# Performance work log

Measured on AMD Instinct MI355X. Metric: run time of the kernel, lower is better.

## Reference

```python
import jax, jax.numpy as jnp
import numpy as np

MAX_N = 32        # mixture degree N
N_PTS = 16384     # number of scalar inputs
INIT_DECAY = 1.0


def setup_inputs() -> dict:
    key = jax.random.key(0)
    k1, _ = jax.random.split(key)
    # inputs assumed elementwise in [-1, 1]
    xs = jax.random.uniform(k1, (N_PTS,), dtype=jnp.float32, minval=-1.0, maxval=1.0)
    # learned logits param, init logits[n] = -n * init_decay (as in __init__)
    logits = -INIT_DECAY * jnp.arange(MAX_N + 1, dtype=jnp.float32)
    return {"xs": xs, "logits": logits}


def _psi(xs, logits, max_n):
    """psi(x) = concat_n sqrt(w_n) * phi_n(x); shape (P, 2*max_n+1).

    phi_0 = [1]; phi_n = [T_n(x), sqrt(1-x^2) * U_{n-1}(x)] for n>=1.
    Single linear-pass recurrence instead of per-degree recompute.
    """
    w = jax.nn.softmax(logits)          # (max_n+1,)
    sw = jnp.sqrt(w)
    xc = jnp.clip(xs, -1.0, 1.0)        # (P,)
    s = jnp.sqrt(jnp.clip(1.0 - xc * xc, 0.0))
    P = xs.shape[0]

    # T_0..T_max_n and U_0..U_max_n via one shared recurrence (fixed small loop)
    Ts = [jnp.ones_like(xc), xc]
    Us = [jnp.ones_like(xc), 2.0 * xc]
    for _ in range(2, max_n + 1):
        Ts.append(2.0 * xc * Ts[-1] - Ts[-2])
        Us.append(2.0 * xc * Us[-1] - Us[-2])
    T = jnp.stack(Ts, axis=-1)          # (P, max_n+1)
    U = jnp.stack(Us, axis=-1)          # (P, max_n+1)

    Tn = T[:, 1:]                       # T_1..T_N            (P, max_n)
    Un = U[:, :max_n]                   # U_0..U_{N-1}        (P, max_n)
    # interleave per degree: [T_n, s * U_{n-1}], weighted by sqrt(w_n)
    pair = jnp.stack([Tn, s[:, None] * Un], axis=-1)   # (P, max_n, 2)
    pair = pair * sw[1:][None, :, None]
    head = sw[0] * jnp.ones((P, 1), dtype=xs.dtype)    # sqrt(w_0) * phi_0
    return jnp.concatenate([head, pair.reshape(P, 2 * max_n)], axis=-1)


def reference(xs, logits):
    """gram(xs) = psi(xs) @ psi(xs)^T, shape (P, P)."""
    psi = _psi(xs, logits, MAX_N)       # (P, 2*MAX_N+1)
    return psi @ psi.T
```

## Files before the change

kernel.cpp:

```cpp
#include <hip/hip_runtime.h>
#include <hip/hip_bf16.h>
#include <math.h>

#define MAXN    32
#define NPTS    16384
#define RSTRIDE 64
#define BTA     32
#define BTB     256
#define NCHUNK  ((BTA + BTB) * RSTRIDE * 2 / 1024)
#define W0_OFF  (NPTS * RSTRIDE)

typedef __attribute__((ext_vector_type(8))) short         bf16x8;
typedef __attribute__((ext_vector_type(4))) float         f32x4;
typedef __attribute__((ext_vector_type(4))) unsigned int  u32x4;

__device__ inline ushort f2bf(float f) {
    union { float f; unsigned u; } v; v.f = f;
    unsigned u = v.u;
    u += 0x7FFFu + ((u >> 16) & 1u);
    return (ushort)(u >> 16);
}

__global__ __launch_bounds__(256) void psi_kernel(
    const float* __restrict__ xs, const float* __restrict__ logits,
    ushort* __restrict__ psi, float* __restrict__ w0scr)
{
    __shared__ ushort srow[256 * RSTRIDE];

    const int tid = threadIdx.x;
    const int pt  = blockIdx.x * 256 + tid;

    float x = xs[pt];
    x = fminf(1.0f, fmaxf(-1.0f, x));
    float s = sqrtf(fmaxf(0.0f, 1.0f - x * x));

    float m = -3.4e38f;
    #pragma unroll
    for (int n = 0; n <= MAXN; ++n) m = fmaxf(m, logits[n]);
    float sum = 0.0f;
    #pragma unroll
    for (int n = 0; n <= MAXN; ++n) sum += __expf(logits[n] - m);
    float inv = 1.0f / sum;

    if (pt == 0) w0scr[0] = __expf(logits[0] - m) * inv;

    ushort tmp[RSTRIDE];
    float Tm1 = 1.0f, T = x;
    float Um1 = 1.0f, U = 2.0f * x;
    float tx = 2.0f * x;
    #pragma unroll
    for (int n = 1; n <= MAXN; ++n) {
        float swn = sqrtf(__expf(logits[n] - m) * inv);
        tmp[2 * n - 2] = f2bf(swn * T);
        tmp[2 * n - 1] = f2bf(swn * (s * Um1));
        float Tn = tx * T - Tm1; Tm1 = T; T = Tn;
        float Un = tx * U - Um1; Um1 = U; U = Un;
    }

    {
        u32x4* lrow = (u32x4*)(srow + tid * RSTRIDE);
        const u32x4* src = (const u32x4*)tmp;
        const int rx = tid & 7;
        #pragma unroll
        for (int j = 0; j < 8; ++j) lrow[j ^ rx] = src[j];
    }
    __syncthreads();

    {
        const u32x4* ls = (const u32x4*)srow;
        u32x4* gd = (u32x4*)(psi + (size_t)blockIdx.x * 256 * RSTRIDE);
        #pragma unroll
        for (int i = 0; i < 8; ++i) gd[i * 256 + tid] = ls[i * 256 + tid];
    }
}

__device__ inline void load_lds16(const void* g, void* l) {
    __builtin_amdgcn_global_load_lds(
        (const __attribute__((address_space(1))) unsigned*)g,
        (__attribute__((address_space(3))) unsigned*)l, 16, 0, 0);
}

__global__ __launch_bounds__(256, 4) void gram_kernel(
    const ushort* __restrict__ psi, const float* __restrict__ w0scr,
    float* __restrict__ out)
{
    __shared__ float ldsF[NCHUNK * 256];

    const int tid  = threadIdx.x;
    const int w    = tid >> 6;
    const int lane = tid & 63;
    const int lr   = lane & 15;
    const int lh   = lane >> 4;
    const int r7   = lr & 7;
    const int bi   = blockIdx.y;
    const int bj   = blockIdx.x;

    const float w0 = w0scr[0];

    {
        const char* gA = (const char*)(psi + (size_t)bi * BTA * RSTRIDE);
        const char* gB = (const char*)(psi + (size_t)bj * BTB * RSTRIDE);
        char* lbase = (char*)ldsF;
        for (int q = w; q < NCHUNK; q += 4) {
            const char* src = (q < 4) ? (gA + q * 1024) : (gB + (q - 4) * 1024);
            load_lds16(src + lane * 16, lbase + q * 1024);
        }
    }
    __syncthreads();

    const char* aPanel = (const char*)ldsF;
    const char* bPanel = (const char*)ldsF + 4096;

    f32x4 acc[2][4];
    #pragma unroll
    for (int rt = 0; rt < 2; ++rt)
        #pragma unroll
        for (int ct = 0; ct < 4; ++ct) acc[rt][ct] = (f32x4){w0, w0, w0, w0};

    #pragma unroll
    for (int ks = 0; ks < 2; ++ks) {
        const int sx = ((ks * 4 + lh) ^ r7) * 16;
        bf16x8 a0 = *(const bf16x8*)(aPanel + (lr      ) * 128 + sx);
        bf16x8 a1 = *(const bf16x8*)(aPanel + (16 + lr ) * 128 + sx);
        #pragma unroll
        for (int ct = 0; ct < 4; ++ct) {
            bf16x8 b = *(const bf16x8*)(bPanel + (w * 64 + ct * 16 + lr) * 128 + sx);
            acc[0][ct] = __builtin_amdgcn_mfma_f32_16x16x32_bf16(b, a0, acc[0][ct], 0, 0, 0);
            acc[1][ct] = __builtin_amdgcn_mfma_f32_16x16x32_bf16(b, a1, acc[1][ct], 0, 0, 0);
        }
    }

    __syncthreads();
    {
        #pragma unroll
        for (int rt = 0; rt < 2; ++rt) {
            const int row = rt * 16 + lr;
            const int rxe = (row & 7) << 2;
            #pragma unroll
            for (int ct = 0; ct < 4; ++ct) {
                int col = (w * 64 + ct * 16 + lh * 4) ^ rxe;
                *(f32x4*)(ldsF + row * BTB + col) = acc[rt][ct];
            }
        }
    }
    __syncthreads();

    {
        #pragma unroll
        for (int p = 0; p < 8; ++p) {
            int row  = p * 4 + w;
            int colr = (lane * 4) ^ ((row & 7) << 2);
            f32x4 v = *(const f32x4*)(ldsF + row * BTB + colr);
            float* dst = out + (size_t)(bi * BTA + row) * NPTS + (size_t)bj * BTB + lane * 4;
            *(f32x4*)dst = v;
        }
    }
}

extern "C" void kernel_launch(void* const* d_in, const int* in_sizes, int n_in,
                              void* d_out, int out_size, void* d_ws, size_t ws_size,
                              hipStream_t stream) {
    const float* xs     = (const float*)d_in[0];
    const float* logits = (const float*)d_in[1];
    float* out          = (float*)d_out;
    ushort* psi         = (ushort*)d_ws;
    float*  w0scr       = (float*)((char*)d_ws + (size_t)W0_OFF * 2);

    psi_kernel<<<NPTS / 256, 256, 0, stream>>>(xs, logits, psi, w0scr);

    dim3 grid(NPTS / BTB, NPTS / BTA);
    gram_kernel<<<grid, 256, 0, stream>>>(psi, w0scr, out);
}
```

Before: 182.4 us.

## Make gram blocks persistent over row tiles with double-buffered A panel

Replaces the 2D grid of small tiles with 512 blocks. Each block loads one 256-column B panel into LDS once, then loops over 64 row tiles of 32 rows. The next A panel is prefetched into a second LDS buffer while the current tile is computed and stored. The aim is to stop reloading the B panel for every tile and to cut per-block launch overhead. In exchange, LDS use per block grows, occupancy drops to 2 blocks per CU, and a barrier per tile may limit how many output stores are in flight on this write-bound kernel.

```diff
diff --git a/kernel.cpp b/kernel.cpp
--- a/kernel.cpp
+++ b/kernel.cpp
@@ -7,8 +7,11 @@
 #define RSTRIDE 64
 #define BTA     32
 #define BTB     256
-#define NCHUNK  ((BTA + BTB) * RSTRIDE * 2 / 1024)
+#define NTILE   64
 #define W0_OFF  (NPTS * RSTRIDE)
+#define B_OFF   0
+#define A_OFF   32768
+#define T_OFF   40960
 
 typedef __attribute__((ext_vector_type(8))) short         bf16x8;
 typedef __attribute__((ext_vector_type(4))) float         f32x4;
@@ -80,11 +83,12 @@
         (__attribute__((address_space(3))) unsigned*)l, 16, 0, 0);
 }
 
-__global__ __launch_bounds__(256, 4) void gram_kernel(
+__global__ __launch_bounds__(256, 2) void gram_kernel(
     const ushort* __restrict__ psi, const float* __restrict__ w0scr,
     float* __restrict__ out)
 {
-    __shared__ float ldsF[NCHUNK * 256];
+    __shared__ float ldsFa[73728 / 4];
+    char* ldsc = (char*)ldsFa;
 
     const int tid  = threadIdx.x;
     const int w    = tid >> 6;
@@ -92,46 +96,53 @@
     const int lr   = lane & 15;
     const int lh   = lane >> 4;
     const int r7   = lr & 7;
-    const int bi   = blockIdx.y;
-    const int bj   = blockIdx.x;
+    const int bid  = blockIdx.x;
+    const int bj   = bid & 63;
+    const int sub  = bid >> 6;
 
     const float w0 = w0scr[0];
 
     {
-        const char* gA = (const char*)(psi + (size_t)bi * BTA * RSTRIDE);
         const char* gB = (const char*)(psi + (size_t)bj * BTB * RSTRIDE);
-        char* lbase = (char*)ldsF;
-        for (int q = w; q < NCHUNK; q += 4) {
-            const char* src = (q < 4) ? (gA + q * 1024) : (gB + (q - 4) * 1024);
-            load_lds16(src + lane * 16, lbase + q * 1024);
-        }
-    }
-    __syncthreads();
-
-    const char* aPanel = (const char*)ldsF;
-    const char* bPanel = (const char*)ldsF + 4096;
-
-    f32x4 acc[2][4];
-    #pragma unroll
-    for (int rt = 0; rt < 2; ++rt)
-        #pragma unroll
-        for (int ct = 0; ct < 4; ++ct) acc[rt][ct] = (f32x4){w0, w0, w0, w0};
-
-    #pragma unroll
-    for (int ks = 0; ks < 2; ++ks) {
-        const int sx = ((ks * 4 + lh) ^ r7) * 16;
-        bf16x8 a0 = *(const bf16x8*)(aPanel + (lr      ) * 128 + sx);
-        bf16x8 a1 = *(const bf16x8*)(aPanel + (16 + lr ) * 128 + sx);
-        #pragma unroll
-        for (int ct = 0; ct < 4; ++ct) {
-            bf16x8 b = *(const bf16x8*)(bPanel + (w * 64 + ct * 16 + lr) * 128 + sx);
-            acc[0][ct] = __builtin_amdgcn_mfma_f32_16x16x32_bf16(b, a0, acc[0][ct], 0, 0, 0);
-            acc[1][ct] = __builtin_amdgcn_mfma_f32_16x16x32_bf16(b, a1, acc[1][ct], 0, 0, 0);
-        }
+        for (int q = w; q < 32; q += 4)
+            load_lds16(gB + q * 1024 + lane * 16, ldsc + B_OFF + q * 1024);
+        const char* gA0 = (const char*)psi + (size_t)(sub * NTILE) * (BTA * RSTRIDE * 2);
+        load_lds16(gA0 + w * 1024 + lane * 16, ldsc + A_OFF + w * 1024);
+        asm volatile("s_waitcnt vmcnt(0)" ::: "memory");
+        __builtin_amdgcn_s_barrier();
     }
 
-    __syncthreads();
-    {
+    const char* bPanel = ldsc + B_OFF;
+    float* tile = (float*)(ldsc + T_OFF);
+
+    int cur = 0;
+    for (int t = 0; t < NTILE; ++t) {
+        const char* aPanel = ldsc + A_OFF + cur * 4096;
+        f32x4 acc[2][4];
+        #pragma unroll
+        for (int rt = 0; rt < 2; ++rt)
+            #pragma unroll
+            for (int ct = 0; ct < 4; ++ct) acc[rt][ct] = (f32x4){w0, w0, w0, w0};
+
+        #pragma unroll
+        for (int ks = 0; ks < 2; ++ks) {
+            const int sx = ((ks * 4 + lh) ^ r7) * 16;
+            bf16x8 a0 = *(const bf16x8*)(aPanel + lr * 128 + sx);
+            bf16x8 a1 = *(const bf16x8*)(aPanel + (16 + lr) * 128 + sx);
+            #pragma unroll
+            for (int ct = 0; ct < 4; ++ct) {
+                bf16x8 b = *(const bf16x8*)(bPanel + (w * 64 + ct * 16 + lr) * 128 + sx);
+                acc[0][ct] = __builtin_amdgcn_mfma_f32_16x16x32_bf16(b, a0, acc[0][ct], 0, 0, 0);
+                acc[1][ct] = __builtin_amdgcn_mfma_f32_16x16x32_bf16(b, a1, acc[1][ct], 0, 0, 0);
+            }
+        }
+
+        if (t < NTILE - 1) {
+            const char* gA = (const char*)psi
+                           + (size_t)(sub * NTILE + t + 1) * (BTA * RSTRIDE * 2);
+            load_lds16(gA + w * 1024 + lane * 16, ldsc + A_OFF + (cur ^ 1) * 4096 + w * 1024);
+        }
+
         #pragma unroll
         for (int rt = 0; rt < 2; ++rt) {
             const int row = rt * 16 + lr;
@@ -139,21 +150,30 @@
             #pragma unroll
             for (int ct = 0; ct < 4; ++ct) {
                 int col = (w * 64 + ct * 16 + lh * 4) ^ rxe;
-                *(f32x4*)(ldsF + row * BTB + col) = acc[rt][ct];
+                *(f32x4*)(tile + row * BTB + col) = acc[rt][ct];
             }
         }
-    }
-    __syncthreads();
+        asm volatile("s_waitcnt lgkmcnt(0)" ::: "memory");
+        __builtin_amdgcn_s_barrier();
 
-    {
-        #pragma unroll
-        for (int p = 0; p < 8; ++p) {
-            int row  = p * 4 + w;
-            int colr = (lane * 4) ^ ((row & 7) << 2);
-            f32x4 v = *(const f32x4*)(ldsF + row * BTB + colr);
-            float* dst = out + (size_t)(bi * BTA + row) * NPTS + (size_t)bj * BTB + lane * 4;
-            *(f32x4*)dst = v;
+        {
+            const size_t rowbase = (size_t)(sub * NTILE + t) * BTA;
+            #pragma unroll
+            for (int p = 0; p < 8; ++p) {
+                int row  = p * 4 + w;
+                int colr = (lane * 4) ^ ((row & 7) << 2);
+                f32x4 v = *(const f32x4*)(tile + row * BTB + colr);
+                float* dst = out + (rowbase + row) * (size_t)NPTS
+                           + (size_t)bj * BTB + lane * 4;
+                *(f32x4*)dst = v;
+            }
         }
+
+        if (t < NTILE - 1) {
+            asm volatile("s_waitcnt vmcnt(8)" ::: "memory");
+            __builtin_amdgcn_s_barrier();
+        }
+        cur ^= 1;
     }
 }
 
@@ -168,6 +188,5 @@
 
     psi_kernel<<<NPTS / 256, 256, 0, stream>>>(xs, logits, psi, w0scr);
 
-    dim3 grid(NPTS / BTB, NPTS / BTA);
-    gram_kernel<<<grid, 256, 0, stream>>>(psi, w0scr, out);
+    gram_kernel<<<512, 256, 0, stream>>>(psi, w0scr, out);
 }
```

Result: slower. 196.8 us (+7.9%).
